# Kernel tuning notes

Measured on AMD Instinct MI355X. Metric: run time of the kernel, lower is better.

The kernel has to match this reference:

```python
import jax, jax.numpy as jnp
import numpy as np

G, N, E, B = 4, 100000, 500000, 512
V, D, H, C = 50000, 300, 128, 20
NUM_HEADS, STEPS = 3, 2


def setup_inputs() -> dict:
    key = jax.random.key(0)
    ks = jax.random.split(key, 12)
    return {
        "node_indices": jax.random.randint(ks[0], (G, N), 0, V),
        "src": jax.random.randint(ks[1], (G, E), 0, N),
        "dst": jax.random.randint(ks[2], (G, E), 0, N),
        "node_graph_ids": jnp.sort(jax.random.randint(ks[3], (G, N), 0, B), axis=-1),
        "edge_weights": jax.random.uniform(ks[4], (G, E), dtype=jnp.float32),
        "emb_table": jax.random.normal(ks[5], (V, D), dtype=jnp.float32) * 0.1,
        "edge_params": jnp.ones((G,), dtype=jnp.float32),
        "W_proj": jax.random.normal(ks[6], (G, D, H), dtype=jnp.float32) / np.sqrt(D),
        "b_proj": jnp.zeros((G, H), dtype=jnp.float32),
        "W_cls": jax.random.normal(ks[7], (G, H, C), dtype=jnp.float32) / np.sqrt(H),
        "b_cls": jnp.zeros((G, C), dtype=jnp.float32),
        "W_fuse": jax.random.normal(ks[8], (NUM_HEADS, C, C, G), dtype=jnp.float32) / np.sqrt(C * G),
        "b_fuse": jnp.zeros((NUM_HEADS, C), dtype=jnp.float32),
    }


def _per_graph_logits(idx, s, d, gid, ew, emb_table, ep, Wp, bp, Wc, bc):
    # embedding lookup + input projection: [N, H]
    h = emb_table[idx] @ Wp + bp
    # graph_learning: relu(scalar * edge_weights)
    w = jax.nn.relu(ep * ew)  # [E]
    # in-degree for DGL mean reduce (0 in-edges -> 0 agg)
    deg = jax.ops.segment_sum(jnp.ones_like(ew), d, num_segments=N)
    inv_deg = jnp.where(deg > 0, 1.0 / deg, 0.0)[:, None]  # [N, 1]
    for _ in range(STEPS):
        msg = h[s] * w[:, None]                                   # gather-multiply [E, H]
        agg = jax.ops.segment_sum(msg, d, num_segments=N) * inv_deg  # scatter-mean [N, H]
        h = h + agg
    # dgl.mean_nodes: per-document mean of node features
    cnt = jax.ops.segment_sum(jnp.ones((N,), h.dtype), gid, num_segments=B)
    doc = jax.ops.segment_sum(h, gid, num_segments=B) / jnp.maximum(cnt, 1.0)[:, None]  # [B, H]
    # classify (dropout = identity in eval)
    return jax.nn.relu(doc) @ Wc + bc  # [B, C]


def reference(node_indices, src, dst, node_graph_ids, edge_weights, emb_table,
              edge_params, W_proj, b_proj, W_cls, b_cls, W_fuse, b_fuse):
    per_graph = jax.vmap(_per_graph_logits,
                         in_axes=(0, 0, 0, 0, 0, None, 0, 0, 0, 0, 0))
    logits = per_graph(node_indices, src, dst, node_graph_ids, edge_weights,
                       emb_table, edge_params, W_proj, b_proj, W_cls, b_cls)  # [G, B, C]
    stacked = jnp.transpose(logits, (1, 2, 0))  # [B, C_in, G] (Conv1d input, kernel=G)
    # Conv1d(out=C, in=C, k=G) per head, valid -> length 1, squeezed
    head_out = jnp.einsum('big,hoig->hbo', stacked, W_fuse) + b_fuse[:, None, :]  # [NH, B, C]
    fused_logits = head_out.mean(axis=0)  # [B, C]
    predictions = jax.nn.softmax(fused_logits, axis=-1)
    return predictions, fused_logits
```

## Files before the change

### kernel.cpp

```cpp
#include <hip/hip_runtime.h>

#define G_  4
#define N_  100000
#define E_  500000
#define B_  512
#define V_  50000
#define D_  300
#define H_  128
#define C_  20
#define NH_ 3

#define KP_  320
#define SCB_  512
#define NBLK_ ((N_ + SCB_ - 1) / SCB_)

typedef unsigned short ushort_t;
typedef __attribute__((ext_vector_type(8))) short bf16x8;
typedef __attribute__((ext_vector_type(4))) float f32x4;

__device__ __forceinline__ ushort_t f2bf(float f) {
    unsigned int x = __float_as_uint(f);
    unsigned int r = x + 0x7FFFu + ((x >> 16) & 1u);
    return (ushort_t)(r >> 16);
}

__device__ __forceinline__ int lower_bound_i(const int* __restrict__ a, int n, int v) {
    int lo = 0, hi = n;
    while (lo < hi) {
        int mid = (lo + hi) >> 1;
        if (a[mid] < v) lo = mid + 1; else hi = mid;
    }
    return lo;
}

__device__ __forceinline__ void unpack8(uint4 u, float* f) {
    f[0] = __uint_as_float((u.x & 0xFFFFu) << 16);
    f[1] = __uint_as_float(u.x & 0xFFFF0000u);
    f[2] = __uint_as_float((u.y & 0xFFFFu) << 16);
    f[3] = __uint_as_float(u.y & 0xFFFF0000u);
    f[4] = __uint_as_float((u.z & 0xFFFFu) << 16);
    f[5] = __uint_as_float(u.z & 0xFFFF0000u);
    f[6] = __uint_as_float((u.w & 0xFFFFu) << 16);
    f[7] = __uint_as_float(u.w & 0xFFFF0000u);
}

__global__ __launch_bounds__(256) void convert_w_kernel(
    const float* __restrict__ Wp,
    ushort_t* __restrict__ Wt)
{
    int flat = blockIdx.x * 256 + threadIdx.x;
    int g = flat / (H_ * KP_);
    int r = flat % (H_ * KP_);
    int n = r / KP_;
    int k = r % KP_;
    float v = (k < D_) ? Wp[((size_t)g * D_ + k) * H_ + n] : 0.f;
    Wt[flat] = f2bf(v);
}

template <int NG>
__global__ __launch_bounds__(256) void mfma_gemm_multi_kernel(
    const float* __restrict__ emb,
    const ushort_t* __restrict__ Wt,
    const float* __restrict__ bp,
    ushort_t* __restrict__ Ph)
{
    const int w    = threadIdx.x >> 6;
    const int l    = threadIdx.x & 63;
    const int l16  = l & 15;
    const int lk   = (l >> 4) * 8;
    const int rb   = blockIdx.x * 64 + (w & 1) * 32;
    const int ch   = (w >> 1) * 64;

    f32x4 acc[NG][2][4];
#pragma unroll
    for (int g = 0; g < NG; ++g)
#pragma unroll
        for (int m = 0; m < 2; ++m)
#pragma unroll
            for (int n = 0; n < 4; ++n) acc[g][m][n] = (f32x4){0.f, 0.f, 0.f, 0.f};

    int arow[2];
    arow[0] = min(rb + l16,      V_ - 1);
    arow[1] = min(rb + 16 + l16, V_ - 1);

    auto load_a = [&](int kb, bf16x8* a) {
#pragma unroll
        for (int m = 0; m < 2; ++m) {
            float v[8];
            const float* ap = &emb[(size_t)arow[m] * D_ + kb];
            if (kb + 8 <= D_) {
                float4 x0 = *reinterpret_cast<const float4*>(ap);
                float4 x1 = *reinterpret_cast<const float4*>(ap + 4);
                v[0] = x0.x; v[1] = x0.y; v[2] = x0.z; v[3] = x0.w;
                v[4] = x1.x; v[5] = x1.y; v[6] = x1.z; v[7] = x1.w;
            } else {
#pragma unroll
                for (int j = 0; j < 8; ++j)
                    v[j] = (kb + j < D_) ? ap[j] : 0.f;
            }
#pragma unroll
            for (int j = 0; j < 8; ++j) a[m][j] = (short)f2bf(v[j]);
        }
    };

    bf16x8 aCur[2], aNxt[2];
    load_a(lk, aCur);

    for (int kp0 = 0; kp0 < KP_; kp0 += 32) {
        const int kb = kp0 + lk;
        if (kp0 + 32 < KP_) load_a(kb + 32, aNxt);

#pragma unroll
        for (int g = 0; g < NG; ++g) {
            const ushort_t* Wg = Wt + (size_t)g * H_ * KP_;
            bf16x8 b[4];
#pragma unroll
            for (int n = 0; n < 4; ++n)
                b[n] = *reinterpret_cast<const bf16x8*>(
                    &Wg[(size_t)(ch + n * 16 + l16) * KP_ + kb]);
#pragma unroll
            for (int m = 0; m < 2; ++m)
#pragma unroll
                for (int n = 0; n < 4; ++n)
                    acc[g][m][n] = __builtin_amdgcn_mfma_f32_16x16x32_bf16(
                        aCur[m], b[n], acc[g][m][n], 0, 0, 0);
        }
        aCur[0] = aNxt[0];
        aCur[1] = aNxt[1];
    }

    const int rbase = (l >> 4) * 4;
#pragma unroll
    for (int g = 0; g < NG; ++g) {
        ushort_t* Pg = Ph + (size_t)g * V_ * H_;
#pragma unroll
        for (int n = 0; n < 4; ++n) {
            const int col  = ch + n * 16 + l16;
            const float bv = bp[g * H_ + col];
#pragma unroll
            for (int m = 0; m < 2; ++m) {
#pragma unroll
                for (int r = 0; r < 4; ++r) {
                    int row = rb + m * 16 + rbase + r;
                    if (row < V_)
                        Pg[(size_t)row * H_ + col] = f2bf(acc[g][m][n][r] + bv);
                }
            }
        }
    }
}

__global__ __launch_bounds__(256) void deg_count_kernel(const int* __restrict__ dstA,
                                                        int* __restrict__ deg)
{
    const int g = blockIdx.y;
    int e = blockIdx.x * 256 + threadIdx.x;
    if (e < E_) atomicAdd(&deg[g * N_ + dstA[(size_t)g * E_ + e]], 1);
}

__global__ __launch_bounds__(512) void scan1_kernel(const int* __restrict__ deg,
                                                    int* __restrict__ bsum)
{
    __shared__ int sh[512];
    const int g = blockIdx.y, b = blockIdx.x, t = threadIdx.x;
    int i = b * SCB_ + t;
    sh[t] = (i < N_) ? deg[g * N_ + i] : 0;
    __syncthreads();
#pragma unroll
    for (int ofs = 256; ofs > 0; ofs >>= 1) {
        if (t < ofs) sh[t] += sh[t + ofs];
        __syncthreads();
    }
    if (t == 0) bsum[g * NBLK_ + b] = sh[0];
}

__global__ __launch_bounds__(256) void scan2_kernel(const int* __restrict__ bsum,
                                                    int* __restrict__ bpre,
                                                    int* __restrict__ off)
{
    __shared__ int sh[256];
    const int g = blockIdx.x, t = threadIdx.x;
    int v = (t < NBLK_) ? bsum[g * NBLK_ + t] : 0;
    sh[t] = v;
    __syncthreads();
#pragma unroll
    for (int ofs = 1; ofs < 256; ofs <<= 1) {
        int u = (t >= ofs) ? sh[t - ofs] : 0;
        __syncthreads();
        sh[t] += u;
        __syncthreads();
    }
    if (t < NBLK_) bpre[g * (NBLK_ + 1) + t + 1] = sh[t];
    if (t == 0) {
        bpre[g * (NBLK_ + 1)] = 0;
        off[(size_t)g * (N_ + 1) + N_] = sh[NBLK_ - 1];
    }
}

__global__ __launch_bounds__(512) void scan3_kernel(int* __restrict__ deg,
                                                    const int* __restrict__ bpre,
                                                    int* __restrict__ off)
{
    __shared__ int sh[512];
    const int g = blockIdx.y, b = blockIdx.x, t = threadIdx.x;
    int i = b * SCB_ + t;
    int v = (i < N_) ? deg[g * N_ + i] : 0;
    sh[t] = v;
    __syncthreads();
#pragma unroll
    for (int ofs = 1; ofs < 512; ofs <<= 1) {
        int u = (t >= ofs) ? sh[t - ofs] : 0;
        __syncthreads();
        sh[t] += u;
        __syncthreads();
    }
    if (i < N_) {
        off[(size_t)g * (N_ + 1) + i] = bpre[g * (NBLK_ + 1) + b] + sh[t] - v;
        deg[g * N_ + i] = 0;
    }
}

__global__ __launch_bounds__(256) void scatter_kernel(
    const int* __restrict__ srcA, const int* __restrict__ dstA,
    const float* __restrict__ ewA, const float* __restrict__ ep,
    const int* __restrict__ idxA, const int* __restrict__ off,
    int* __restrict__ cnt, int4* __restrict__ csr4)
{
    const int g = blockIdx.y;
    int e = blockIdx.x * 256 + threadIdx.x;
    if (e >= E_) return;
    int s = srcA[(size_t)g * E_ + e];
    int d = dstA[(size_t)g * E_ + e];
    int pos = off[(size_t)g * (N_ + 1) + d] + atomicAdd(&cnt[g * N_ + d], 1);
    float w = ep[g] * ewA[(size_t)g * E_ + e];
    csr4[(size_t)g * E_ + pos] =
        make_int4(s, idxA[(size_t)g * N_ + s], __float_as_int(fmaxf(w, 0.f)), 0);
}

__global__ __launch_bounds__(256) void prop1_kernel(
    const int* __restrict__ idx_g, const int* __restrict__ off,
    const int4* __restrict__ csr4,
    const ushort_t* __restrict__ Ph, ushort_t* __restrict__ hBh)
{
    const int n = blockIdx.x * 16 + (threadIdx.x >> 4);
    if (n >= N_) return;
    const int lane = threadIdx.x & 15;
    const int col  = lane * 8;

    const int lo = off[n], hi = off[n + 1];

    float sf[8];
    unpack8(*reinterpret_cast<const uint4*>(&Ph[(size_t)idx_g[n] * H_ + col]), sf);

    float acc[8];
#pragma unroll
    for (int j = 0; j < 8; ++j) acc[j] = 0.f;

    int i = lo;
    for (; i + 4 <= hi; i += 4) {
        int4 e0 = csr4[i],     e1 = csr4[i + 1];
        int4 e2 = csr4[i + 2], e3 = csr4[i + 3];
        float c0 = __int_as_float(e0.z), c1 = __int_as_float(e1.z);
        float c2 = __int_as_float(e2.z), c3 = __int_as_float(e3.z);
        uint4 u0 = *reinterpret_cast<const uint4*>(&Ph[(size_t)e0.y * H_ + col]);
        uint4 u1 = *reinterpret_cast<const uint4*>(&Ph[(size_t)e1.y * H_ + col]);
        uint4 u2 = *reinterpret_cast<const uint4*>(&Ph[(size_t)e2.y * H_ + col]);
        uint4 u3 = *reinterpret_cast<const uint4*>(&Ph[(size_t)e3.y * H_ + col]);
        float f0[8], f1[8], f2[8], f3[8];
        unpack8(u0, f0); unpack8(u1, f1); unpack8(u2, f2); unpack8(u3, f3);
#pragma unroll
        for (int j = 0; j < 8; ++j)
            acc[j] += c0 * f0[j] + c1 * f1[j] + c2 * f2[j] + c3 * f3[j];
    }
    for (; i < hi; ++i) {
        int4 e0 = csr4[i];
        float c = __int_as_float(e0.z);
        float f[8];
        unpack8(*reinterpret_cast<const uint4*>(&Ph[(size_t)e0.y * H_ + col]), f);
#pragma unroll
        for (int j = 0; j < 8; ++j) acc[j] += c * f[j];
    }

    const float inv = (hi > lo) ? 1.0f / (float)(hi - lo) : 0.f;
    ushort_t p[8];
#pragma unroll
    for (int j = 0; j < 8; ++j) p[j] = f2bf(sf[j] + inv * acc[j]);
    uint4 o;
    o.x = (unsigned)p[0] | ((unsigned)p[1] << 16);
    o.y = (unsigned)p[2] | ((unsigned)p[3] << 16);
    o.z = (unsigned)p[4] | ((unsigned)p[5] << 16);
    o.w = (unsigned)p[6] | ((unsigned)p[7] << 16);
    *reinterpret_cast<uint4*>(&hBh[(size_t)n * H_ + col]) = o;
}

__global__ __launch_bounds__(256) void prop2_fused_kernel(
    const int* __restrict__ off, const int4* __restrict__ csr4,
    const int* __restrict__ gid,
    const ushort_t* __restrict__ hBh, float* __restrict__ docsum)
{
    const int nloc = threadIdx.x >> 4;
    const int n    = blockIdx.x * 16 + nloc;
    const int lane = threadIdx.x & 15;
    const int col  = lane * 8;

    __shared__ float sh[16][H_];
    __shared__ int   shgid[16];

    float o[8];
    if (n < N_) {
        const int lo = off[n], hi = off[n + 1];

        float sf[8];
        unpack8(*reinterpret_cast<const uint4*>(&hBh[(size_t)n * H_ + col]), sf);

        float acc[8];
#pragma unroll
        for (int j = 0; j < 8; ++j) acc[j] = 0.f;

        int i = lo;
        for (; i + 4 <= hi; i += 4) {
            int4 e0 = csr4[i],     e1 = csr4[i + 1];
            int4 e2 = csr4[i + 2], e3 = csr4[i + 3];
            float c0 = __int_as_float(e0.z), c1 = __int_as_float(e1.z);
            float c2 = __int_as_float(e2.z), c3 = __int_as_float(e3.z);
            uint4 u0 = *reinterpret_cast<const uint4*>(&hBh[(size_t)e0.x * H_ + col]);
            uint4 u1 = *reinterpret_cast<const uint4*>(&hBh[(size_t)e1.x * H_ + col]);
            uint4 u2 = *reinterpret_cast<const uint4*>(&hBh[(size_t)e2.x * H_ + col]);
            uint4 u3 = *reinterpret_cast<const uint4*>(&hBh[(size_t)e3.x * H_ + col]);
            float f0[8], f1[8], f2[8], f3[8];
            unpack8(u0, f0); unpack8(u1, f1); unpack8(u2, f2); unpack8(u3, f3);
#pragma unroll
            for (int j = 0; j < 8; ++j)
                acc[j] += c0 * f0[j] + c1 * f1[j] + c2 * f2[j] + c3 * f3[j];
        }
        for (; i < hi; ++i) {
            int4 e0 = csr4[i];
            float c = __int_as_float(e0.z);
            float f[8];
            unpack8(*reinterpret_cast<const uint4*>(&hBh[(size_t)e0.x * H_ + col]), f);
#pragma unroll
            for (int j = 0; j < 8; ++j) acc[j] += c * f[j];
        }

        const float inv = (hi > lo) ? 1.0f / (float)(hi - lo) : 0.f;
#pragma unroll
        for (int j = 0; j < 8; ++j) o[j] = sf[j] + inv * acc[j];
        if (lane == 0) shgid[nloc] = gid[n];
    } else {
#pragma unroll
        for (int j = 0; j < 8; ++j) o[j] = 0.f;
        if (lane == 0) shgid[nloc] = -1;
    }

#pragma unroll
    for (int j = 0; j < 8; ++j) sh[nloc][col + j] = o[j];
    __syncthreads();

    const int c  = threadIdx.x & 127;
    const int q  = threadIdx.x >> 7;
    const int n0 = q * 8;
    float run = 0.f;
    int rgid = shgid[n0];
    for (int k = 0; k < 8; ++k) {
        int gk = shgid[n0 + k];
        if (gk != rgid) {
            if (rgid >= 0) atomicAdd(&docsum[(size_t)rgid * H_ + c], run);
            run = 0.f; rgid = gk;
        }
        run += sh[n0 + k][c];
    }
    if (rgid >= 0) atomicAdd(&docsum[(size_t)rgid * H_ + c], run);
}

__global__ __launch_bounds__(128) void cls_kernel(
    const int* __restrict__ gidA, const float* __restrict__ docsum,
    const float* __restrict__ Wc, const float* __restrict__ bc,
    float* __restrict__ logits)
{
    const int b   = blockIdx.x;
    const int g   = blockIdx.y;
    const int tid = threadIdx.x;
    const int* gid = gidA + (size_t)g * N_;

    int lo = lower_bound_i(gid, N_, b);
    int hi = lower_bound_i(gid, N_, b + 1);
    float cnt = (float)(hi - lo);

    __shared__ float sdoc[H_];
    float dv = docsum[((size_t)g * B_ + b) * H_ + tid] / fmaxf(cnt, 1.0f);
    sdoc[tid] = fmaxf(dv, 0.f);
    __syncthreads();

    if (tid < C_) {
        const float* Wcg = Wc + (size_t)g * H_ * C_;
        float acc = bc[g * C_ + tid];
#pragma unroll 8
        for (int hh = 0; hh < H_; ++hh) acc += sdoc[hh] * Wcg[hh * C_ + tid];
        logits[((size_t)g * B_ + b) * C_ + tid] = acc;
    }
}

__global__ __launch_bounds__(64) void fuse_kernel(
    const float* __restrict__ logits,
    const float* __restrict__ Wf,
    const float* __restrict__ bf,
    float* __restrict__ out)
{
    const int b   = blockIdx.x;
    const int tid = threadIdx.x;

    __shared__ float s[C_ * G_];
    __shared__ float fl[C_];

    for (int t = tid; t < C_ * G_; t += 64) {
        int i = t >> 2, g = t & 3;
        s[t] = logits[((long)g * B_ + b) * C_ + i];
    }
    __syncthreads();

    if (tid < C_) {
        float acc = 0.f;
        for (int hd = 0; hd < NH_; ++hd) {
            float a = bf[hd * C_ + tid];
            const float* wrow = &Wf[((hd * C_ + tid) * C_) * G_];
#pragma unroll 5
        for (int i = 0; i < C_; ++i) {
#pragma unroll
                for (int g = 0; g < G_; ++g)
                    a += s[i * G_ + g] * wrow[i * G_ + g];
            }
            acc += a;
        }
        fl[tid] = acc * (1.0f / 3.0f);
    }
    __syncthreads();

    if (tid < C_) {
        float f = fl[tid];
        float m = -1e30f;
#pragma unroll
        for (int i = 0; i < C_; ++i) m = fmaxf(m, fl[i]);
        float ssum = 0.f;
#pragma unroll
        for (int i = 0; i < C_; ++i) ssum += expf(fl[i] - m);
        out[b * C_ + tid] = expf(f - m) / ssum;
        out[B_ * C_ + b * C_ + tid] = f;
    }
}

extern "C" void kernel_launch(void* const* d_in, const int* in_sizes, int n_in,
                              void* d_out, int out_size, void* d_ws, size_t ws_size,
                              hipStream_t stream)
{
    const int*   node_indices = (const int*)d_in[0];
    const int*   srcA         = (const int*)d_in[1];
    const int*   dstA         = (const int*)d_in[2];
    const int*   gidA         = (const int*)d_in[3];
    const float* ewA          = (const float*)d_in[4];
    const float* emb          = (const float*)d_in[5];
    const float* ep           = (const float*)d_in[6];
    const float* Wp           = (const float*)d_in[7];
    const float* bp           = (const float*)d_in[8];
    const float* Wc           = (const float*)d_in[9];
    const float* bc           = (const float*)d_in[10];
    const float* Wf           = (const float*)d_in[11];
    const float* bf           = (const float*)d_in[12];
    float*       out          = (float*)d_out;

    char* wp0 = (char*)d_ws;
    auto alloc = [&](size_t bytes) {
        void* r = (void*)wp0;
        wp0 += (bytes + 255) & ~(size_t)255;
        return r;
    };
    ushort_t* hBh      = (ushort_t*)alloc((size_t)N_ * H_ * 2);
    float*    docsum   = (float*)   alloc((size_t)G_ * B_ * H_ * 4);
    float*    logits   = (float*)   alloc((size_t)G_ * B_ * C_ * 4);
    ushort_t* Wt       = (ushort_t*)alloc((size_t)G_ * H_ * KP_ * 2);
    int*      deg_i    = (int*)     alloc((size_t)G_ * N_ * 4);
    int*      off      = (int*)     alloc((size_t)G_ * (N_ + 1) * 4);
    int*      bsum     = (int*)     alloc((size_t)G_ * NBLK_ * 4);
    int*      bpre     = (int*)     alloc((size_t)G_ * (NBLK_ + 1) * 4);
    int4*     csr4     = (int4*)    alloc((size_t)G_ * E_ * 16);

    const size_t pbytes = (size_t)V_ * H_ * 2;
    size_t used  = (size_t)(wp0 - (char*)d_ws);
    size_t avail = (ws_size > used) ? ws_size - used : 0;

    int ng;
    if (avail >= 4 * pbytes + 1024)      ng = 4;
    else if (avail >= 2 * pbytes + 1024) ng = 2;
    else                                 ng = 1;
    ushort_t* Ph = (ushort_t*)alloc((size_t)ng * pbytes);

    convert_w_kernel<<<(G_ * H_ * KP_) / 256, 256, 0, stream>>>(Wp, Wt);
    hipMemsetAsync(docsum, 0, (size_t)G_ * B_ * H_ * sizeof(float), stream);

    hipMemsetAsync(deg_i, 0, (size_t)G_ * N_ * sizeof(int), stream);
    deg_count_kernel<<<dim3((E_ + 255) / 256, G_), 256, 0, stream>>>(dstA, deg_i);
    scan1_kernel<<<dim3(NBLK_, G_), 512, 0, stream>>>(deg_i, bsum);
    scan2_kernel<<<G_, 256, 0, stream>>>(bsum, bpre, off);
    scan3_kernel<<<dim3(NBLK_, G_), 512, 0, stream>>>(deg_i, bpre, off);
    scatter_kernel<<<dim3((E_ + 255) / 256, G_), 256, 0, stream>>>(
        srcA, dstA, ewA, ep, node_indices, off, deg_i, csr4);

    const int gemm_blocks = (V_ + 63) / 64;
    for (int gbase = 0; gbase < G_; gbase += ng) {
        const ushort_t* Wtg = Wt + (size_t)gbase * H_ * KP_;
        const float*    bpg = bp + (size_t)gbase * H_;
        if (ng == 4)
            mfma_gemm_multi_kernel<4><<<gemm_blocks, 256, 0, stream>>>(emb, Wtg, bpg, Ph);
        else if (ng == 2)
            mfma_gemm_multi_kernel<2><<<gemm_blocks, 256, 0, stream>>>(emb, Wtg, bpg, Ph);
        else
            mfma_gemm_multi_kernel<1><<<gemm_blocks, 256, 0, stream>>>(emb, Wtg, bpg, Ph);

        for (int gi = 0; gi < ng; ++gi) {
            const int g = gbase + gi;
            const int*      idx   = node_indices + (size_t)g * N_;
            const int*      gid   = gidA + (size_t)g * N_;
            const int*      off_g = off + (size_t)g * (N_ + 1);
            const int4*     csr_g = csr4 + (size_t)g * E_;
            const ushort_t* Pg    = Ph + (size_t)gi * V_ * H_;

            prop1_kernel<<<(N_ + 15) / 16, 256, 0, stream>>>(
                idx, off_g, csr_g, Pg, hBh);
            prop2_fused_kernel<<<(N_ + 15) / 16, 256, 0, stream>>>(
                off_g, csr_g, gid, hBh, docsum + (size_t)g * B_ * H_);
        }
    }

    cls_kernel<<<dim3(B_, G_), 128, 0, stream>>>(gidA, docsum, Wc, bc, logits);
    fuse_kernel<<<B_, 64, 0, stream>>>(logits, Wf, bf, out);
}
```

Measured before the change: 592.3 us.

## Stage embedding rows through shared memory in projection GEMM with smaller row tiles

The projection GEMM now loads each 32-row tile of the embedding table cooperatively into LDS with coalesced float4 loads, then each wave reads its A fragments from LDS. The block tile changes from 64 rows × 128 cols split 2×2 across waves to 32 rows × 128 cols with each wave owning 32 columns, which doubles the block count. The aim is to remove the strided, uncoalesced per-lane global reads of emb and the duplicate reads across waves. In exchange it adds two barriers per k-step and loads W fragments twice as often per output row, and each wave has fewer MFMAs per loop iteration.

```diff
diff --git a/kernel.cpp b/kernel.cpp
--- a/kernel.cpp
+++ b/kernel.cpp
@@ -58,75 +58,86 @@
 }
 
 template <int NG>
-__global__ __launch_bounds__(256) void mfma_gemm_multi_kernel(
+__global__ __launch_bounds__(256) void mfma_gemm_lds_kernel(
     const float* __restrict__ emb,
     const ushort_t* __restrict__ Wt,
     const float* __restrict__ bp,
     ushort_t* __restrict__ Ph)
 {
-    const int w    = threadIdx.x >> 6;
-    const int l    = threadIdx.x & 63;
+    __shared__ float As[32][36];
+
+    const int t    = threadIdx.x;
+    const int w    = t >> 6;
+    const int l    = t & 63;
     const int l16  = l & 15;
     const int lk   = (l >> 4) * 8;
-    const int rb   = blockIdx.x * 64 + (w & 1) * 32;
-    const int ch   = (w >> 1) * 64;
-
-    f32x4 acc[NG][2][4];
+    const int ch   = w * 32;
+    const int rowbase = blockIdx.x * 32;
+
+    const int srow = t >> 3;
+    const int skq  = t & 7;
+    const int grow = min(rowbase + srow, V_ - 1);
+    const float* arow_p = &emb[(size_t)grow * D_];
+
+    auto ldA = [&](int k0) -> float4 {
+        int k = k0 + skq * 4;
+        if (k + 4 <= D_) return *reinterpret_cast<const float4*>(arow_p + k);
+        float4 v = make_float4(0.f, 0.f, 0.f, 0.f);
+        if (k     < D_) v.x = arow_p[k];
+        if (k + 1 < D_) v.y = arow_p[k + 1];
+        if (k + 2 < D_) v.z = arow_p[k + 2];
+        if (k + 3 < D_) v.w = arow_p[k + 3];
+        return v;
+    };
+
+    f32x4 acc[NG][2][2];
 #pragma unroll
     for (int g = 0; g < NG; ++g)
 #pragma unroll
         for (int m = 0; m < 2; ++m)
 #pragma unroll
-            for (int n = 0; n < 4; ++n) acc[g][m][n] = (f32x4){0.f, 0.f, 0.f, 0.f};
-
-    int arow[2];
-    arow[0] = min(rb + l16,      V_ - 1);
-    arow[1] = min(rb + 16 + l16, V_ - 1);
-
-    auto load_a = [&](int kb, bf16x8* a) {
+            for (int n = 0; n < 2; ++n) acc[g][m][n] = (f32x4){0.f, 0.f, 0.f, 0.f};
+
+    float4 pf = ldA(0);
+
+    for (int k0 = 0; k0 < KP_; k0 += 32) {
+        As[srow][skq * 4 + 0] = pf.x;
+        As[srow][skq * 4 + 1] = pf.y;
+        As[srow][skq * 4 + 2] = pf.z;
+        As[srow][skq * 4 + 3] = pf.w;
+        __syncthreads();
+
+        if (k0 + 32 < KP_) pf = ldA(k0 + 32);
+
+        bf16x8 a[2];
 #pragma unroll
         for (int m = 0; m < 2; ++m) {
-            float v[8];
-            const float* ap = &emb[(size_t)arow[m] * D_ + kb];
-            if (kb + 8 <= D_) {
-                float4 x0 = *reinterpret_cast<const float4*>(ap);
-                float4 x1 = *reinterpret_cast<const float4*>(ap + 4);
-                v[0] = x0.x; v[1] = x0.y; v[2] = x0.z; v[3] = x0.w;
-                v[4] = x1.x; v[5] = x1.y; v[6] = x1.z; v[7] = x1.w;
-            } else {
-#pragma unroll
-                for (int j = 0; j < 8; ++j)
-                    v[j] = (kb + j < D_) ? ap[j] : 0.f;
-            }
-#pragma unroll
-            for (int j = 0; j < 8; ++j) a[m][j] = (short)f2bf(v[j]);
-        }
-    };
-
-    bf16x8 aCur[2], aNxt[2];
-    load_a(lk, aCur);
-
-    for (int kp0 = 0; kp0 < KP_; kp0 += 32) {
-        const int kb = kp0 + lk;
-        if (kp0 + 32 < KP_) load_a(kb + 32, aNxt);
-
+            const float* ap = &As[m * 16 + l16][lk];
+            float4 x0 = *reinterpret_cast<const float4*>(ap);
+            float4 x1 = *reinterpret_cast<const float4*>(ap + 4);
+            a[m][0] = (short)f2bf(x0.x); a[m][1] = (short)f2bf(x0.y);
+            a[m][2] = (short)f2bf(x0.z); a[m][3] = (short)f2bf(x0.w);
+            a[m][4] = (short)f2bf(x1.x); a[m][5] = (short)f2bf(x1.y);
+            a[m][6] = (short)f2bf(x1.z); a[m][7] = (short)f2bf(x1.w);
+        }
+
+        const int kb = k0 + lk;
 #pragma unroll
         for (int g = 0; g < NG; ++g) {
             const ushort_t* Wg = Wt + (size_t)g * H_ * KP_;
-            bf16x8 b[4];
-#pragma unroll
-            for (int n = 0; n < 4; ++n)
+            bf16x8 b[2];
+#pragma unroll
+            for (int n = 0; n < 2; ++n)
                 b[n] = *reinterpret_cast<const bf16x8*>(
                     &Wg[(size_t)(ch + n * 16 + l16) * KP_ + kb]);
 #pragma unroll
             for (int m = 0; m < 2; ++m)
 #pragma unroll
-                for (int n = 0; n < 4; ++n)
+                for (int n = 0; n < 2; ++n)
                     acc[g][m][n] = __builtin_amdgcn_mfma_f32_16x16x32_bf16(
-                        aCur[m], b[n], acc[g][m][n], 0, 0, 0);
-        }
-        aCur[0] = aNxt[0];
-        aCur[1] = aNxt[1];
+                        a[m], b[n], acc[g][m][n], 0, 0, 0);
+        }
+        __syncthreads();
     }
 
     const int rbase = (l >> 4) * 4;
@@ -134,14 +145,14 @@
     for (int g = 0; g < NG; ++g) {
         ushort_t* Pg = Ph + (size_t)g * V_ * H_;
 #pragma unroll
-        for (int n = 0; n < 4; ++n) {
+        for (int n = 0; n < 2; ++n) {
             const int col  = ch + n * 16 + l16;
             const float bv = bp[g * H_ + col];
 #pragma unroll
             for (int m = 0; m < 2; ++m) {
 #pragma unroll
                 for (int r = 0; r < 4; ++r) {
-                    int row = rb + m * 16 + rbase + r;
+                    int row = rowbase + m * 16 + rbase + r;
                     if (row < V_)
                         Pg[(size_t)row * H_ + col] = f2bf(acc[g][m][n][r] + bv);
                 }
@@ -504,16 +515,16 @@
     scatter_kernel<<<dim3((E_ + 255) / 256, G_), 256, 0, stream>>>(
         srcA, dstA, ewA, ep, node_indices, off, deg_i, csr4);
 
-    const int gemm_blocks = (V_ + 63) / 64;
+    const int gemm_blocks = (V_ + 31) / 32;
     for (int gbase = 0; gbase < G_; gbase += ng) {
         const ushort_t* Wtg = Wt + (size_t)gbase * H_ * KP_;
         const float*    bpg = bp + (size_t)gbase * H_;
         if (ng == 4)
-            mfma_gemm_multi_kernel<4><<<gemm_blocks, 256, 0, stream>>>(emb, Wtg, bpg, Ph);
+            mfma_gemm_lds_kernel<4><<<gemm_blocks, 256, 0, stream>>>(emb, Wtg, bpg, Ph);
         else if (ng == 2)
-            mfma_gemm_multi_kernel<2><<<gemm_blocks, 256, 0, stream>>>(emb, Wtg, bpg, Ph);
+            mfma_gemm_lds_kernel<2><<<gemm_blocks, 256, 0, stream>>>(emb, Wtg, bpg, Ph);
         else
-            mfma_gemm_multi_kernel<1><<<gemm_blocks, 256, 0, stream>>>(emb, Wtg, bpg, Ph);
+            mfma_gemm_lds_kernel<1><<<gemm_blocks, 256, 0, stream>>>(emb, Wtg, bpg, Ph);
 
         for (int gi = 0; gi < ng; ++gi) {
             const int g = gbase + gi;
```

Result: faster. 533.6 us (-9.9%).
